# Kernel optimization log

Measured on AMD Instinct MI355X. Metric: run time of the kernel, lower is better.

Reference implementation:

```python
import jax, jax.numpy as jnp
import numpy as np

N_AGENTS = 10
N_ENEMIES = 11
N_ALLIES = 9
H = 64           # rnn_hidden_dim
HYP = 64         # api_hyper_dim
DEPTH = 2        # residual_depth
OWN = 32
EF = 10          # enemy_feats_dim
AF = 10          # ally_feats_dim
N_ACTIONS = 17
BS = 1024


def _hypernet(x, win, bin_, wres, bres, wout, bout):
    # Linear -> ReLU -> DEPTH x (ReLU(Linear)+identity) -> Linear
    h = jax.nn.relu(x @ win + bin_)
    for d in range(DEPTH):
        h = jax.nn.relu(h @ wres[d] + bres[d]) + h
    return h @ wout + bout


def _gru_cell(x, h, wi, wh, bi, bh):
    gi = x @ wi + bi
    gh = h @ wh + bh
    ir, iz, in_ = jnp.split(gi, 3, axis=-1)
    hr, hz, hn = jnp.split(gh, 3, axis=-1)
    r = jax.nn.sigmoid(ir + hr)
    z = jax.nn.sigmoid(iz + hz)
    n = jnp.tanh(in_ + r * hn)
    return (1.0 - z) * n + z * h


def setup_inputs() -> dict:
    key = jax.random.key(0)
    ks = iter(jax.random.split(key, 48))
    def p(shape, s=0.1):
        return jax.random.normal(next(ks), shape, jnp.float32) * s
    N = BS * N_AGENTS
    inp = {
        'own_feats':    p((N, OWN), 1.0),
        'enemy_feats':  p((N * N_ENEMIES, EF), 1.0),
        'ally_feats':   p((N * N_ALLIES, AF), 1.0),
        'hidden_state': p((N, H), 1.0),
        'fc1_w': p((OWN, H)), 'fc1_b': p((H,)),
        'agent_emb': p((N_AGENTS, H)), 'action_emb': p((N_ACTIONS, H)),
        'hen_win': p((EF, HYP)), 'hen_bin': p((HYP,)),
        'hen_wres': p((DEPTH, HYP, HYP)), 'hen_bres': p((DEPTH, HYP)),
        'hen_wout': p((HYP, EF * H)), 'hen_bout': p((EF * H,)),
        'hal_win': p((AF, HYP)), 'hal_bin': p((HYP,)),
        'hal_wres': p((DEPTH, HYP, HYP)), 'hal_bres': p((DEPTH, HYP)),
        'hal_wout': p((HYP, AF * H)), 'hal_bout': p((AF * H,)),
        'gru_wi': p((H, 3 * H)), 'gru_wh': p((H, 3 * H)),
        'gru_bi': p((3 * H,)), 'gru_bh': p((3 * H,)),
        'fc2_w': p((H, 6)), 'fc2_b': p((6,)),
        'how_win': p((EF, HYP)), 'how_bin': p((HYP,)),
        'how_wres': p((DEPTH, HYP, HYP)), 'how_bres': p((DEPTH, HYP)),
        'how_wout': p((HYP, H)), 'how_bout': p((H,)),
        'hob_win': p((EF, HYP)), 'hob_bin': p((HYP,)),
        'hob_wres': p((DEPTH, HYP, HYP)), 'hob_bres': p((DEPTH, HYP)),
        'hob_wout': p((HYP, 1)), 'hob_bout': p((1,)),
        'agent_idx': jax.random.randint(next(ks), (N,), 0, N_AGENTS),
        'last_action_idx': jax.random.randint(next(ks), (N,), 0, N_ACTIONS),
        'bs': BS,
    }
    return inp


def reference(own_feats, enemy_feats, ally_feats, hidden_state,
              fc1_w, fc1_b, agent_emb, action_emb,
              hen_win, hen_bin, hen_wres, hen_bres, hen_wout, hen_bout,
              hal_win, hal_bin, hal_wres, hal_bres, hal_wout, hal_bout,
              gru_wi, gru_wh, gru_bi, gru_bh,
              fc2_w, fc2_b,
              how_win, how_bin, how_wres, how_bres, how_wout, how_bout,
              hob_win, hob_bin, hob_wres, hob_bres, hob_wout, hob_bout,
              agent_idx, last_action_idx, bs):
    N = bs * N_AGENTS
    # own embedding + id embeddings
    emb = own_feats @ fc1_w + fc1_b
    emb = emb + agent_emb[agent_idx] + action_emb[last_action_idx]
    # per-enemy hypernet weights [N*NE, EF, H]; bmm + sum-pool over enemies
    w_en = _hypernet(enemy_feats, hen_win, hen_bin, hen_wres, hen_bres,
                     hen_wout, hen_bout).reshape(-1, EF, H)
    emb_en = jnp.einsum('nf,nfh->nh', enemy_feats, w_en)
    emb_en = emb_en.reshape(N, N_ENEMIES, H).sum(axis=1)
    # per-ally hypernet weights + bmm + sum-pool
    w_al = _hypernet(ally_feats, hal_win, hal_bin, hal_wres, hal_bres,
                     hal_wout, hal_bout).reshape(-1, AF, H)
    emb_al = jnp.einsum('nf,nfh->nh', ally_feats, w_al)
    emb_al = emb_al.reshape(N, N_ALLIES, H).sum(axis=1)
    x = jax.nn.relu(emb + emb_en + emb_al)
    hh = _gru_cell(x, hidden_state.reshape(-1, H), gru_wi, gru_wh, gru_bi, gru_bh)
    q_normal = (hh @ fc2_w + fc2_b).reshape(bs, N_AGENTS, 6)
    # attack-action head: hypernet-generated per-enemy weights/biases
    ow = _hypernet(enemy_feats, how_win, how_bin, how_wres, how_bres,
                   how_wout, how_bout).reshape(N, N_ENEMIES, H)
    ob = _hypernet(enemy_feats, hob_win, hob_bin, hob_wres, hob_bres,
                   hob_wout, hob_bout).reshape(N, N_ENEMIES)
    q_attack = (jnp.einsum('nh,neh->ne', hh, ow) + ob).reshape(bs, N_AGENTS, N_ENEMIES)
    q = jnp.concatenate([q_normal, q_attack], axis=-1)
    return q, hh.reshape(bs, N_AGENTS, H)
```

## Files before the change

### kernel.cpp

```cpp
#include <hip/hip_runtime.h>

#define DI static __device__ __forceinline__

typedef short s16x8 __attribute__((ext_vector_type(8)));
typedef float f32x4 __attribute__((ext_vector_type(4)));
typedef unsigned u32x2 __attribute__((ext_vector_type(2)));

DI unsigned short f2b(float f) {
  union { float f; unsigned u; } v; v.f = f;
  return (unsigned short)((v.u + 0x7FFF + ((v.u >> 16) & 1)) >> 16);
}
DI float b2f(unsigned short s) {
  union { unsigned u; float f; } v; v.u = ((unsigned)s) << 16;
  return v.f;
}
DI unsigned cvtpk(float lo, float hi) {
  unsigned r;
  asm("v_cvt_pk_bf16_f32 %0, %1, %2" : "=v"(r) : "v"(lo), "v"(hi));
  return r;
}
DI f32x4 MFMA(s16x8 a, s16x8 b, f32x4 c) {
  return __builtin_amdgcn_mfma_f32_16x16x32_bf16(a, b, c, 0, 0, 0);
}
DI s16x8 ldg8(const unsigned short* p) { return *(const s16x8*)p; }

#define OFF_WEN   0
#define OFF_WAL   10240
#define OFF_WHOW  20480
#define OFF_WHOB  30720
#define OFF_BGEN  40960
#define OFF_BGAL  83968
#define OFF_WIT   126976
#define OFF_WHT   139264
#define OFF_FC1T  151552
#define OFF_FC2E  153600
#define OFF_HOWT  154624
#define SH_END    159744
#define B_EMB_EN  (SH_END*2)
#define B_EMB_AL  (B_EMB_EN + 2621440)
#define B_HB      (B_EMB_AL + 2621440)
#define B_GBF     (B_HB + 40960)

#define PSTR 680
#define HSTR 72
#define XSTR 40

#define SLOT 28160
#define XBC  5632
DI int xoffc(int row, int b) { return ((row*32  + b) ^ ((row & 7) << 4)); }
DI int hoffc(int row, int b) { return XBC + ((row*128 + b) ^ ((row & 7) << 4)); }

__global__ __launch_bounds__(256) void kprep(
    const float* __restrict__ hen_win, const float* __restrict__ hen_wres,
    const float* __restrict__ hal_win, const float* __restrict__ hal_wres,
    const float* __restrict__ how_win, const float* __restrict__ how_wres,
    const float* __restrict__ hob_win, const float* __restrict__ hob_wres,
    const float* __restrict__ hen_wout, const float* __restrict__ hen_bout,
    const float* __restrict__ hal_wout, const float* __restrict__ hal_bout,
    const float* __restrict__ gru_wi, const float* __restrict__ gru_wh,
    const float* __restrict__ fc1_w, const float* __restrict__ fc2_w,
    const float* __restrict__ how_bout, const float* __restrict__ how_wout,
    unsigned short* __restrict__ ws)
{
  const int gid = blockIdx.x * 256 + threadIdx.x;
  const int gsz = gridDim.x * 256;
  for (int i = gid; i < 4 * 10240; i += gsz) {
    int s = i / 10240, idx = i - s * 10240;
    const float* win  = (s == 0) ? hen_win  : (s == 1) ? hal_win  : (s == 2) ? how_win  : hob_win;
    const float* wres = (s == 0) ? hen_wres : (s == 1) ? hal_wres : (s == 2) ? how_wres : hob_wres;
    float v;
    if (idx < 2048) { int n = idx >> 5, k = idx & 31; v = (k < 10) ? win[k*64 + n] : 0.f; }
    else { int r = idx - 2048; int d = r >> 12; int r2 = r & 4095; int n = r2 >> 6, k = r2 & 63;
           v = wres[d*4096 + k*64 + n]; }
    ws[s * 10240 + idx] = f2b(v);
  }
  for (int i = gid; i < 2 * 43008; i += gsz) {
    int s = i / 43008, idx = i - s * 43008;
    const float* wout = s ? hal_wout : hen_wout;
    const float* bout = s ? hal_bout : hen_bout;
    int kl = idx & 31, n = (idx >> 5) & 63, c = idx >> 11;
    int kfg = c * 32 + kl;
    float v = 0.f;
    if (kfg < 640)      { int k = kfg / 10, f = kfg - k * 10; v = wout[k*640 + f*64 + n]; }
    else if (kfg < 650) { v = bout[(kfg - 640)*64 + n]; }
    ws[(s ? OFF_BGAL : OFF_BGEN) + idx] = f2b(v);
  }
  for (int i = gid; i < 2 * 12288; i += gsz) {
    int s = i / 12288, idx = i - s * 12288;
    int n = idx >> 6, k = idx & 63;
    const float* w = s ? gru_wh : gru_wi;
    ws[(s ? OFF_WHT : OFF_WIT) + idx] = f2b(w[k*192 + n]);
  }
  for (int i = gid; i < 2048; i += gsz) { int n = i >> 5, k = i & 31; ws[OFF_FC1T + i] = f2b(fc1_w[k*64 + n]); }
  for (int i = gid; i < 1024; i += gsz) {
    int n = i >> 6, k = i & 63;
    float v = 0.f; if (n < 6) v = fc2_w[k*6 + n]; else if (n == 6) v = how_bout[k];
    ws[OFF_FC2E + i] = f2b(v);
  }
  for (int i = gid; i < 4096; i += gsz) ws[OFF_HOWT + i] = f2b(how_wout[i]);
}

DI void stage_item(const float* __restrict__ feats, int vrows, char* sl) {
  for (int idx = threadIdx.x; idx < 176*16; idx += 256) {
    int row = idx >> 4, c = idx & 15;
    float v = (row < vrows && c < 10) ? feats[row*10 + c] : 0.f;
    *(unsigned short*)(sl + xoffc(row, c*2)) = f2b(v);
  }
}

DI void stackP(char* sl, int ntiles, const unsigned short* __restrict__ wg,
               const float* __restrict__ bin, const float* __restrict__ bres)
{
  const int l = threadIdx.x & 63, wv = threadIdx.x >> 6;
  const int lrow = l & 15, gq = l >> 4, lk8 = gq * 8;
  const int tis[3] = {wv, wv + 4, wv + 8};
  f32x4 hval[3][4];
  {
    s16x8 wf[4]; f32x4 bv[4];
#pragma unroll
    for (int mt = 0; mt < 4; mt++) {
      wf[mt] = ldg8(wg + (mt*16 + lrow)*32 + lk8);
      bv[mt] = *(const f32x4*)(bin + mt*16 + gq*4);
    }
#pragma unroll
    for (int tt = 0; tt < 3; tt++) {
      if (tis[tt] < ntiles) {
        int row = tis[tt]*16 + lrow;
        s16x8 xf = *(const s16x8*)(sl + xoffc(row, gq*16));
#pragma unroll
        for (int mt = 0; mt < 4; mt++) {
          f32x4 d = MFMA(wf[mt], xf, bv[mt]);
#pragma unroll
          for (int r = 0; r < 4; r++) hval[tt][mt][r] = fmaxf(d[r], 0.f);
          u32x2 pw; pw.x = cvtpk(hval[tt][mt][0], hval[tt][mt][1]);
          pw.y = cvtpk(hval[tt][mt][2], hval[tt][mt][3]);
          *(u32x2*)(sl + hoffc(row, (mt*16 + gq*4)*2)) = pw;
        }
      }
    }
  }
#pragma unroll
  for (int d = 0; d < 2; d++) {
    const unsigned short* wt = wg + 2048 + d * 4096;
    s16x8 wf0[4], wf1[4]; f32x4 bv[4];
#pragma unroll
    for (int mt = 0; mt < 4; mt++) {
      wf0[mt] = ldg8(wt + (mt*16 + lrow)*64 + lk8);
      wf1[mt] = ldg8(wt + (mt*16 + lrow)*64 + 32 + lk8);
      bv[mt] = *(const f32x4*)(bres + d*64 + mt*16 + gq*4);
    }
#pragma unroll
    for (int tt = 0; tt < 3; tt++) {
      if (tis[tt] < ntiles) {
        int row = tis[tt]*16 + lrow;
        s16x8 b0 = *(const s16x8*)(sl + hoffc(row, gq*16));
        s16x8 b1 = *(const s16x8*)(sl + hoffc(row, 64 + gq*16));
#pragma unroll
        for (int mt = 0; mt < 4; mt++) {
          f32x4 acc = MFMA(wf0[mt], b0, bv[mt]);
          acc = MFMA(wf1[mt], b1, acc);
#pragma unroll
          for (int r = 0; r < 4; r++)
            hval[tt][mt][r] = fmaxf(acc[r], 0.f) + hval[tt][mt][r];
          u32x2 pw; pw.x = cvtpk(hval[tt][mt][0], hval[tt][mt][1]);
          pw.y = cvtpk(hval[tt][mt][2], hval[tt][mt][3]);
          *(u32x2*)(sl + hoffc(row, (mt*16 + gq*4)*2)) = pw;
        }
      }
    }
  }
}

__global__ __launch_bounds__(256) void khyp_ea(
    const float* __restrict__ en_feats, const float* __restrict__ al_feats,
    const unsigned short* __restrict__ ws,
    const float* __restrict__ en_bin, const float* __restrict__ en_bres,
    const float* __restrict__ al_bin, const float* __restrict__ al_bres,
    float* __restrict__ emb_en, float* __restrict__ emb_al)
{
  __shared__ __align__(16) char smem[2*SLOT];
  const int t = threadIdx.x;
  const int l = t & 63, wv = t >> 6;
  const int lrow = l & 15, gq = l >> 4, lk8 = gq * 8;

  int its[3]; int nit = 0;
  for (int it = blockIdx.x; it < 1280; it += 512) its[nit++] = it;

  {
    int it0 = its[0];
    const float* f0 = (it0 < 640) ? en_feats + (long)it0*1760
                                  : al_feats + (long)(it0-640)*1440;
    stage_item(f0, (it0 < 640) ? 176 : 144, smem);
  }
  __syncthreads();

  for (int i = 0; i < nit; i++) {
    char* sl = smem + (i & 1) * SLOT;
    const int it = its[i];
    const bool en = it < 640;
    const int E = en ? 11 : 9;
    const float* feats = en ? en_feats + (long)it*1760 : al_feats + (long)(it-640)*1440;
    const unsigned short* Wg = ws + (en ? OFF_WEN : OFF_WAL);
    const unsigned short* Bg = ws + (en ? OFF_BGEN : OFF_BGAL);
    const float* bin  = en ? en_bin  : al_bin;
    const float* bres = en ? en_bres : al_bres;
    float* emb = en ? emb_en + (long)it*1024 : emb_al + (long)(it-640)*1024;

    stackP(sl, E, Wg, bin, bres);
    __syncthreads();

    const int a = t >> 4, kq = t & 15, k0 = kq * 4;
    float acc[4][10];
#pragma unroll
    for (int kk = 0; kk < 4; kk++)
#pragma unroll
      for (int f = 0; f < 10; f++) acc[kk][f] = 0.f;
    for (int e = 0; e < E; e++) {
      int row = a * E + e;
      s16x8 xv8 = *(const s16x8*)(sl + xoffc(row, 0));
      unsigned xv2 = *(const unsigned*)(sl + xoffc(row, 16));
      float xf[10];
#pragma unroll
      for (int f = 0; f < 8; f++) xf[f] = b2f((unsigned short)xv8[f]);
      xf[8] = b2f((unsigned short)(xv2 & 0xFFFF));
      xf[9] = b2f((unsigned short)(xv2 >> 16));
      u32x2 hp = *(const u32x2*)(sl + hoffc(row, k0*2));
      float hf[4] = { b2f((unsigned short)(hp.x & 0xFFFF)), b2f((unsigned short)(hp.x >> 16)),
                      b2f((unsigned short)(hp.y & 0xFFFF)), b2f((unsigned short)(hp.y >> 16)) };
#pragma unroll
      for (int kk = 0; kk < 4; kk++)
#pragma unroll
        for (int f = 0; f < 10; f++) acc[kk][f] += hf[kk] * xf[f];
    }
    float sxv = 0.f; int a2 = 0, fx = 0;
    if (t < 160) {
      a2 = t / 10; fx = t - a2 * 10;
      for (int e = 0; e < E; e++) sxv += feats[(a2*E + e)*10 + fx];
    }
    __syncthreads();

    unsigned short* P2 = (unsigned short*)sl;
    {
      unsigned* Pw = (unsigned*)(P2 + a*PSTR + k0*10);
#pragma unroll
      for (int m = 0; m < 20; m++) {
        const int v0 = 2*m, v1 = 2*m + 1;
        Pw[m] = cvtpk(acc[v0/10][v0%10], acc[v1/10][v1%10]);
      }
    }
    if (t < 160) P2[a2*PSTR + 640 + fx] = f2b(sxv);
    if (t < 352) { int a3 = t / 22, c = t - a3*22; P2[a3*PSTR + 650 + c] = 0; }
    if (i + 1 < nit) {
      int itn = its[i+1];
      const float* fn = (itn < 640) ? en_feats + (long)itn*1760
                                    : al_feats + (long)(itn-640)*1440;
      stage_item(fn, (itn < 640) ? 176 : 144, smem + ((i+1) & 1) * SLOT);
    }
    __syncthreads();

    f32x4 g0 = {0.f,0.f,0.f,0.f}, g1 = {0.f,0.f,0.f,0.f};
    const unsigned short* Bw = Bg + (wv*16 + lrow)*32 + lk8;
#pragma unroll
    for (int c = 0; c < 21; c++) {
      s16x8 af = *(const s16x8*)&P2[lrow*PSTR + c*32 + lk8];
      s16x8 bf = ldg8(Bw + c*2048);
      if (c & 1) g1 = MFMA(af, bf, g1); else g0 = MFMA(af, bf, g0);
    }
#pragma unroll
    for (int r = 0; r < 4; r++)
      emb[(gq*4 + r)*64 + wv*16 + lrow] = g0[r] + g1[r];
  }
}

__global__ __launch_bounds__(256) void kfused(
    const float* __restrict__ own, const float* __restrict__ agent_emb,
    const float* __restrict__ action_emb,
    const int* __restrict__ agent_idx, const int* __restrict__ last_action,
    const float* __restrict__ emb_en, const float* __restrict__ emb_al,
    const float* __restrict__ hidden,
    const unsigned short* __restrict__ ws,
    const float* __restrict__ fc1_b, const float* __restrict__ bi,
    const float* __restrict__ bh, const float* __restrict__ fc2_b,
    float* __restrict__ qout, float* __restrict__ hhout,
    unsigned short* __restrict__ g_bf, float* __restrict__ hb)
{
  __shared__ unsigned short own_lds[16*32];
  __shared__ unsigned short x_lds[16*HSTR];
  __shared__ unsigned short hp_lds[16*HSTR];
  __shared__ unsigned short hh_lds[16*HSTR];
  const int t = threadIdx.x;
  const int l = t & 63, wv = t >> 6;
  const int lrow = l & 15, lk8 = (l >> 4) * 8, lr4 = (l >> 4) * 4;
  const int n0 = blockIdx.x * 16;

  const unsigned short* fc1T = ws + OFF_FC1T;
  const unsigned short* wiT  = ws + OFF_WIT;
  const unsigned short* whT  = ws + OFF_WHT;
  const unsigned short* howT = ws + OFF_HOWT;
  const unsigned short* fc2e = ws + OFF_FC2E;

  for (int i = t; i < 512; i += 256) own_lds[i] = f2b(own[n0*32 + i]);
  for (int i = t; i < 1024; i += 256) hp_lds[(i >> 6)*HSTR + (i & 63)] = f2b(hidden[n0*64 + i]);
  __syncthreads();

  const int j = wv * 16 + lrow;
  {
    s16x8 a0 = *(const s16x8*)&own_lds[lrow*32 + lk8];
    s16x8 b0 = ldg8(fc1T + (wv*16 + lrow)*32 + lk8);
    f32x4 c0 = MFMA(a0, b0, f32x4{0.f,0.f,0.f,0.f});
    float fb = fc1_b[j];
#pragma unroll
    for (int r = 0; r < 4; r++) {
      int aa = lr4 + r; int n = n0 + aa;
      int ai = agent_idx[n], la = last_action[n];
      float v = c0[r] + fb + agent_emb[ai*64 + j] + action_emb[la*64 + j]
              + emb_en[(long)n*64 + j] + emb_al[(long)n*64 + j];
      x_lds[aa*HSTR + j] = f2b(fmaxf(v, 0.f));
    }
  }
  __syncthreads();

  {
    s16x8 xa[2], ha[2];
#pragma unroll
    for (int s = 0; s < 2; s++) {
      xa[s] = *(const s16x8*)&x_lds[lrow*HSTR + s*32 + lk8];
      ha[s] = *(const s16x8*)&hp_lds[lrow*HSTR + s*32 + lk8];
    }
    f32x4 gi[3], gh[3];
#pragma unroll
    for (int g3 = 0; g3 < 3; g3++) { gi[g3] = f32x4{0.f,0.f,0.f,0.f}; gh[g3] = f32x4{0.f,0.f,0.f,0.f}; }
#pragma unroll
    for (int g3 = 0; g3 < 3; g3++) {
      int tl = wv + g3 * 4;
#pragma unroll
      for (int s = 0; s < 2; s++) {
        gi[g3] = MFMA(xa[s], ldg8(wiT + (tl*16 + lrow)*64 + s*32 + lk8), gi[g3]);
        gh[g3] = MFMA(ha[s], ldg8(whT + (tl*16 + lrow)*64 + s*32 + lk8), gh[g3]);
      }
    }
    float bir = bi[j], biz = bi[64 + j], bin_ = bi[128 + j];
    float bhr = bh[j], bhz = bh[64 + j], bhn = bh[128 + j];
#pragma unroll
    for (int r = 0; r < 4; r++) {
      int aa = lr4 + r; int n = n0 + aa;
      float rr = 1.f / (1.f + __expf(-(gi[0][r] + bir + gh[0][r] + bhr)));
      float zz = 1.f / (1.f + __expf(-(gi[1][r] + biz + gh[1][r] + bhz)));
      float nn = tanhf(gi[2][r] + bin_ + rr * (gh[2][r] + bhn));
      float hp = hidden[n*64 + j];
      float hhv = (1.f - zz) * nn + zz * hp;
      hhout[n*64 + j] = hhv;
      hh_lds[aa*HSTR + j] = f2b(hhv);
    }
  }
  __syncthreads();

  {
    s16x8 hha[2];
#pragma unroll
    for (int s = 0; s < 2; s++) hha[s] = *(const s16x8*)&hh_lds[lrow*HSTR + s*32 + lk8];
    f32x4 gc = {0.f,0.f,0.f,0.f};
#pragma unroll
    for (int s = 0; s < 2; s++) gc = MFMA(hha[s], ldg8(howT + (wv*16 + lrow)*64 + s*32 + lk8), gc);
#pragma unroll
    for (int r = 0; r < 4; r++) g_bf[(n0 + lr4 + r)*64 + wv*16 + lrow] = f2b(gc[r]);
    if (wv == 0) {
      f32x4 qc = {0.f,0.f,0.f,0.f};
#pragma unroll
      for (int s = 0; s < 2; s++) qc = MFMA(hha[s], ldg8(fc2e + lrow*64 + s*32 + lk8), qc);
#pragma unroll
      for (int r = 0; r < 4; r++) {
        int n = n0 + lr4 + r;
        if (lrow < 6)       qout[n*17 + lrow] = qc[r] + fc2_b[lrow];
        else if (lrow == 6) hb[n] = qc[r];
      }
    }
  }
}

template<int TMAX, bool WLAST>
DI void stack_batch(const unsigned short* __restrict__ x_lds,
                    unsigned short* const (&hbp)[TMAX], const int (&tis)[TMAX], int NT,
                    const unsigned short* __restrict__ wg,
                    const float* __restrict__ bin, const float* __restrict__ bres,
                    f32x4 (&hval)[TMAX][4])
{
  const int l = threadIdx.x & 63;
  const int lrow = l & 15, gq = l >> 4, lk8 = gq * 8;
  {
    s16x8 wf[4]; f32x4 bv[4];
#pragma unroll
    for (int mt = 0; mt < 4; mt++) {
      wf[mt] = ldg8(wg + (mt*16 + lrow)*32 + lk8);
      bv[mt] = *(const f32x4*)(bin + mt*16 + gq*4);
    }
#pragma unroll
    for (int tt = 0; tt < TMAX; tt++) {
      if (tis[tt] < NT) {
        s16x8 xf = *(const s16x8*)&x_lds[(tis[tt]*16 + lrow)*XSTR + lk8];
#pragma unroll
        for (int mt = 0; mt < 4; mt++) {
          f32x4 d = MFMA(wf[mt], xf, bv[mt]);
#pragma unroll
          for (int r = 0; r < 4; r++) hval[tt][mt][r] = fmaxf(d[r], 0.f);
        }
        unsigned short* wr = hbp[tt] + lrow*HSTR;
#pragma unroll
        for (int mt = 0; mt < 4; mt++) {
          u32x2 pw;
          pw.x = cvtpk(hval[tt][mt][0], hval[tt][mt][1]);
          pw.y = cvtpk(hval[tt][mt][2], hval[tt][mt][3]);
          *(u32x2*)&wr[mt*16 + gq*4] = pw;
        }
      }
    }
  }
#pragma unroll
  for (int d = 0; d < 2; d++) {
    const unsigned short* wt = wg + 2048 + d * 4096;
    s16x8 wf[4][2]; f32x4 bv[4];
#pragma unroll
    for (int mt = 0; mt < 4; mt++) {
      wf[mt][0] = ldg8(wt + (mt*16 + lrow)*64 + lk8);
      wf[mt][1] = ldg8(wt + (mt*16 + lrow)*64 + 32 + lk8);
      bv[mt] = *(const f32x4*)(bres + d*64 + mt*16 + gq*4);
    }
#pragma unroll
    for (int tt = 0; tt < TMAX; tt++) {
      if (tis[tt] < NT) {
        const unsigned short* hr = hbp[tt] + lrow*HSTR;
        s16x8 b0 = *(const s16x8*)&hr[lk8];
        s16x8 b1 = *(const s16x8*)&hr[32 + lk8];
#pragma unroll
        for (int mt = 0; mt < 4; mt++) {
          f32x4 a = MFMA(wf[mt][0], b0, bv[mt]);
          a = MFMA(wf[mt][1], b1, a);
#pragma unroll
          for (int r = 0; r < 4; r++)
            hval[tt][mt][r] = fmaxf(a[r], 0.f) + hval[tt][mt][r];
        }
        if (d == 0 || WLAST) {
          unsigned short* wr = hbp[tt] + lrow*HSTR;
#pragma unroll
          for (int mt = 0; mt < 4; mt++) {
            u32x2 pw;
            pw.x = cvtpk(hval[tt][mt][0], hval[tt][mt][1]);
            pw.y = cvtpk(hval[tt][mt][2], hval[tt][mt][3]);
            *(u32x2*)&wr[mt*16 + gq*4] = pw;
          }
        }
      }
    }
  }
}

__global__ __launch_bounds__(256) void kattack(
    const float* __restrict__ en_feats, const unsigned short* __restrict__ ws,
    const float* __restrict__ how_bin, const float* __restrict__ how_bres,
    const float* __restrict__ hob_bin, const float* __restrict__ hob_bres,
    const unsigned short* __restrict__ g_bf, const float* __restrict__ hbuf,
    const float* __restrict__ hob_wout, const float* __restrict__ hob_bout,
    float* __restrict__ qout)
{
  __shared__ __align__(16) char smem[41728];
  unsigned short* x_lds = (unsigned short*)smem;
  unsigned short* scr   = (unsigned short*)(smem + 14080);
  const int t = threadIdx.x;
  const int l = t & 63, wv = t >> 6;
  const int lrow = l & 15, gq = l >> 4;
  const int blk = blockIdx.x;
  const float* feats = en_feats + (long)blk * 1760;

  for (int idx = t; idx < 176*32; idx += 256) {
    int row = idx >> 5, c = idx & 31;
    x_lds[row*XSTR + c] = (c < 10) ? f2b(feats[row*10 + c]) : (unsigned short)0;
  }
  __syncthreads();

  int tis[3] = {wv, wv + 4, wv + 8};
  unsigned short* hbp[3] = { scr + (wv*3+0)*16*HSTR, scr + (wv*3+1)*16*HSTR, scr + (wv*3+2)*16*HSTR };
  f32x4 hval[3][4];

  stack_batch<3, false>(x_lds, hbp, tis, 11, ws + OFF_WHOB, hob_bin, hob_bres, hval);
  f32x4 hw[4];
#pragma unroll
  for (int mt = 0; mt < 4; mt++) hw[mt] = *(const f32x4*)(hob_wout + mt*16 + gq*4);
  float qbv[3] = {0.f, 0.f, 0.f};
#pragma unroll
  for (int tt = 0; tt < 3; tt++) {
    if (tis[tt] < 11) {
      float s = 0.f;
#pragma unroll
      for (int mt = 0; mt < 4; mt++)
#pragma unroll
        for (int r = 0; r < 4; r++) s += hval[tt][mt][r] * hw[mt][r];
      s += __shfl_xor(s, 16, 64);
      s += __shfl_xor(s, 32, 64);
      qbv[tt] = s;
    }
  }

  stack_batch<3, false>(x_lds, hbp, tis, 11, ws + OFF_WHOW, how_bin, how_bres, hval);
  const float hob_b0 = hob_bout[0];
#pragma unroll
  for (int tt = 0; tt < 3; tt++) {
    if (tis[tt] < 11) {
      int row = tis[tt]*16 + lrow;
      unsigned ag = (unsigned)row / 11u;
      int n = blk*16 + (int)ag;
      float s = 0.f;
#pragma unroll
      for (int mt = 0; mt < 4; mt++) {
        u32x2 gv = *(const u32x2*)(g_bf + (long)n*64 + mt*16 + gq*4);
        s += hval[tt][mt][0] * b2f((unsigned short)(gv.x & 0xFFFF))
           + hval[tt][mt][1] * b2f((unsigned short)(gv.x >> 16))
           + hval[tt][mt][2] * b2f((unsigned short)(gv.y & 0xFFFF))
           + hval[tt][mt][3] * b2f((unsigned short)(gv.y >> 16));
      }
      s += __shfl_xor(s, 16, 64);
      s += __shfl_xor(s, 32, 64);
      if (l < 16) {
        int e = row - (int)ag * 11;
        qout[n*17 + 6 + e] = s + qbv[tt] + hbuf[n] + hob_b0;
      }
    }
  }
}

extern "C" void kernel_launch(void* const* d_in, const int* in_sizes, int n_in,
                              void* d_out, int out_size, void* d_ws, size_t ws_size,
                              hipStream_t stream)
{
  (void)in_sizes; (void)n_in; (void)out_size; (void)ws_size;
  const float* own        = (const float*)d_in[0];
  const float* enemy      = (const float*)d_in[1];
  const float* ally       = (const float*)d_in[2];
  const float* hidden     = (const float*)d_in[3];
  const float* fc1_w      = (const float*)d_in[4];
  const float* fc1_b      = (const float*)d_in[5];
  const float* agent_emb  = (const float*)d_in[6];
  const float* action_emb = (const float*)d_in[7];
  const float* hen_win  = (const float*)d_in[8];  const float* hen_bin  = (const float*)d_in[9];
  const float* hen_wres = (const float*)d_in[10]; const float* hen_bres = (const float*)d_in[11];
  const float* hen_wout = (const float*)d_in[12]; const float* hen_bout = (const float*)d_in[13];
  const float* hal_win  = (const float*)d_in[14]; const float* hal_bin  = (const float*)d_in[15];
  const float* hal_wres = (const float*)d_in[16]; const float* hal_bres = (const float*)d_in[17];
  const float* hal_wout = (const float*)d_in[18]; const float* hal_bout = (const float*)d_in[19];
  const float* gru_wi = (const float*)d_in[20];   const float* gru_wh = (const float*)d_in[21];
  const float* gru_bi = (const float*)d_in[22];   const float* gru_bh = (const float*)d_in[23];
  const float* fc2_w  = (const float*)d_in[24];   const float* fc2_b  = (const float*)d_in[25];
  const float* how_win  = (const float*)d_in[26]; const float* how_bin  = (const float*)d_in[27];
  const float* how_wres = (const float*)d_in[28]; const float* how_bres = (const float*)d_in[29];
  const float* how_wout = (const float*)d_in[30]; const float* how_bout = (const float*)d_in[31];
  const float* hob_win  = (const float*)d_in[32]; const float* hob_bin  = (const float*)d_in[33];
  const float* hob_wres = (const float*)d_in[34]; const float* hob_bres = (const float*)d_in[35];
  const float* hob_wout = (const float*)d_in[36]; const float* hob_bout = (const float*)d_in[37];
  const int* agent_idx   = (const int*)d_in[38];
  const int* last_action = (const int*)d_in[39];

  unsigned short* ws = (unsigned short*)d_ws;
  float* emb_en = (float*)((char*)d_ws + B_EMB_EN);
  float* emb_al = (float*)((char*)d_ws + B_EMB_AL);
  float* hb     = (float*)((char*)d_ws + B_HB);
  unsigned short* g_bf = (unsigned short*)((char*)d_ws + B_GBF);

  float* q  = (float*)d_out;
  float* hh = q + 1024*10*17;

  kprep<<<128, 256, 0, stream>>>(hen_win, hen_wres, hal_win, hal_wres,
      how_win, how_wres, hob_win, hob_wres,
      hen_wout, hen_bout, hal_wout, hal_bout,
      gru_wi, gru_wh, fc1_w, fc2_w, how_bout, how_wout, ws);
  khyp_ea<<<512, 256, 0, stream>>>(enemy, ally, ws,
      hen_bin, hen_bres, hal_bin, hal_bres, emb_en, emb_al);
  kfused<<<640, 256, 0, stream>>>(own, agent_emb, action_emb, agent_idx, last_action,
      emb_en, emb_al, hidden, ws, fc1_b, gru_bi, gru_bh, fc2_b, q, hh, g_bf, hb);
  kattack<<<640, 256, 0, stream>>>(enemy, ws, how_bin, how_bres, hob_bin, hob_bres,
      g_bf, hb, hob_wout, hob_bout, q);
}
```

Measured before the change: 78.05 us.

## Process two fixed items per block in khyp_ea, sharing weight fragments

The khyp_ea kernel changes from a grid-stride loop over 1280 items with 512 blocks (unbalanced: 2 or 3 items per block) to 640 blocks that each handle exactly two items of the same type, enemy or ally. Each hypernet weight fragment is loaded once and applied to both items, and the final 21-step MFMA loop reuses each B fragment for two accumulators. The cost is more live registers (hval doubled) and the loss of overlap between staging the next item and computing the current one.

```diff
diff --git a/kernel.cpp b/kernel.cpp
--- a/kernel.cpp
+++ b/kernel.cpp
@@ -108,67 +108,54 @@
   }
 }
 
-DI void stackP(char* sl, int ntiles, const unsigned short* __restrict__ wg,
-               const float* __restrict__ bin, const float* __restrict__ bres)
-{
-  const int l = threadIdx.x & 63, wv = threadIdx.x >> 6;
-  const int lrow = l & 15, gq = l >> 4, lk8 = gq * 8;
-  const int tis[3] = {wv, wv + 4, wv + 8};
-  f32x4 hval[3][4];
-  {
-    s16x8 wf[4]; f32x4 bv[4];
-#pragma unroll
-    for (int mt = 0; mt < 4; mt++) {
-      wf[mt] = ldg8(wg + (mt*16 + lrow)*32 + lk8);
-      bv[mt] = *(const f32x4*)(bin + mt*16 + gq*4);
-    }
-#pragma unroll
-    for (int tt = 0; tt < 3; tt++) {
-      if (tis[tt] < ntiles) {
-        int row = tis[tt]*16 + lrow;
-        s16x8 xf = *(const s16x8*)(sl + xoffc(row, gq*16));
-#pragma unroll
-        for (int mt = 0; mt < 4; mt++) {
-          f32x4 d = MFMA(wf[mt], xf, bv[mt]);
-#pragma unroll
-          for (int r = 0; r < 4; r++) hval[tt][mt][r] = fmaxf(d[r], 0.f);
-          u32x2 pw; pw.x = cvtpk(hval[tt][mt][0], hval[tt][mt][1]);
-          pw.y = cvtpk(hval[tt][mt][2], hval[tt][mt][3]);
-          *(u32x2*)(sl + hoffc(row, (mt*16 + gq*4)*2)) = pw;
-        }
-      }
-    }
-  }
-#pragma unroll
-  for (int d = 0; d < 2; d++) {
-    const unsigned short* wt = wg + 2048 + d * 4096;
-    s16x8 wf0[4], wf1[4]; f32x4 bv[4];
-#pragma unroll
-    for (int mt = 0; mt < 4; mt++) {
-      wf0[mt] = ldg8(wt + (mt*16 + lrow)*64 + lk8);
-      wf1[mt] = ldg8(wt + (mt*16 + lrow)*64 + 32 + lk8);
-      bv[mt] = *(const f32x4*)(bres + d*64 + mt*16 + gq*4);
-    }
-#pragma unroll
-    for (int tt = 0; tt < 3; tt++) {
-      if (tis[tt] < ntiles) {
-        int row = tis[tt]*16 + lrow;
-        s16x8 b0 = *(const s16x8*)(sl + hoffc(row, gq*16));
-        s16x8 b1 = *(const s16x8*)(sl + hoffc(row, 64 + gq*16));
-#pragma unroll
-        for (int mt = 0; mt < 4; mt++) {
-          f32x4 acc = MFMA(wf0[mt], b0, bv[mt]);
-          acc = MFMA(wf1[mt], b1, acc);
-#pragma unroll
-          for (int r = 0; r < 4; r++)
-            hval[tt][mt][r] = fmaxf(acc[r], 0.f) + hval[tt][mt][r];
-          u32x2 pw; pw.x = cvtpk(hval[tt][mt][0], hval[tt][mt][1]);
-          pw.y = cvtpk(hval[tt][mt][2], hval[tt][mt][3]);
-          *(u32x2*)(sl + hoffc(row, (mt*16 + gq*4)*2)) = pw;
-        }
-      }
-    }
-  }
+DI void pbuild_acc(const char* sl, int E, float (&acc)[4][10]) {
+  const int t = threadIdx.x;
+  const int a = t >> 4, k0 = (t & 15) * 4;
+#pragma unroll
+  for (int kk = 0; kk < 4; kk++)
+#pragma unroll
+    for (int f = 0; f < 10; f++) acc[kk][f] = 0.f;
+  for (int e = 0; e < E; e++) {
+    int row = a * E + e;
+    s16x8 xv8 = *(const s16x8*)(sl + xoffc(row, 0));
+    unsigned xv2 = *(const unsigned*)(sl + xoffc(row, 16));
+    float xf[10];
+#pragma unroll
+    for (int f = 0; f < 8; f++) xf[f] = b2f((unsigned short)xv8[f]);
+    xf[8] = b2f((unsigned short)(xv2 & 0xFFFF));
+    xf[9] = b2f((unsigned short)(xv2 >> 16));
+    u32x2 hp = *(const u32x2*)(sl + hoffc(row, k0*2));
+    float hf[4] = { b2f((unsigned short)(hp.x & 0xFFFF)), b2f((unsigned short)(hp.x >> 16)),
+                    b2f((unsigned short)(hp.y & 0xFFFF)), b2f((unsigned short)(hp.y >> 16)) };
+#pragma unroll
+    for (int kk = 0; kk < 4; kk++)
+#pragma unroll
+      for (int f = 0; f < 10; f++) acc[kk][f] += hf[kk] * xf[f];
+  }
+}
+
+DI void pbuild_write(unsigned short* P2, const float (&acc)[4][10], float sxv, int E,
+                     const float* __restrict__ feats) {
+  const int t = threadIdx.x;
+  const int a = t >> 4, k0 = (t & 15) * 4;
+  unsigned* Pw = (unsigned*)(P2 + a*PSTR + k0*10);
+#pragma unroll
+  for (int m = 0; m < 20; m++) {
+    const int v0 = 2*m, v1 = 2*m + 1;
+    Pw[m] = cvtpk(acc[v0/10][v0%10], acc[v1/10][v1%10]);
+  }
+  if (t < 160) { int a2 = t / 10, fx = t - a2*10; P2[a2*PSTR + 640 + fx] = f2b(sxv); }
+  if (t < 352) { int a3 = t / 22, c = t - a3*22; P2[a3*PSTR + 650 + c] = 0; }
+}
+
+DI float sx_of(const float* __restrict__ feats, int E) {
+  const int t = threadIdx.x;
+  float s = 0.f;
+  if (t < 160) {
+    int a2 = t / 10, fx = t - a2 * 10;
+    for (int e = 0; e < E; e++) s += feats[(a2*E + e)*10 + fx];
+  }
+  return s;
 }
 
 __global__ __launch_bounds__(256) void khyp_ea(
@@ -183,92 +170,119 @@
   const int l = t & 63, wv = t >> 6;
   const int lrow = l & 15, gq = l >> 4, lk8 = gq * 8;
 
-  int its[3]; int nit = 0;
-  for (int it = blockIdx.x; it < 1280; it += 512) its[nit++] = it;
-
+  const bool en = blockIdx.x < 320;
+  const int i0 = en ? blockIdx.x * 2 : (blockIdx.x - 320) * 2;
+  const int E = en ? 11 : 9;
+  const int rows = E * 16;
+  const float* feats0 = (en ? en_feats : al_feats) + (long)i0 * rows * 10;
+  const float* feats1 = feats0 + rows * 10;
+  const unsigned short* Wg = ws + (en ? OFF_WEN : OFF_WAL);
+  const unsigned short* Bg = ws + (en ? OFF_BGEN : OFF_BGAL);
+  const float* bin  = en ? en_bin  : al_bin;
+  const float* bres = en ? en_bres : al_bres;
+  float* emb0 = (en ? emb_en : emb_al) + (long)i0 * 1024;
+  float* emb1 = emb0 + 1024;
+
+  stage_item(feats0, rows, smem);
+  stage_item(feats1, rows, smem + SLOT);
+  __syncthreads();
+
+  const int tis[3] = {wv, wv + 4, wv + 8};
+  f32x4 hval[2][3][4];
   {
-    int it0 = its[0];
-    const float* f0 = (it0 < 640) ? en_feats + (long)it0*1760
-                                  : al_feats + (long)(it0-640)*1440;
-    stage_item(f0, (it0 < 640) ? 176 : 144, smem);
-  }
-  __syncthreads();
-
-  for (int i = 0; i < nit; i++) {
-    char* sl = smem + (i & 1) * SLOT;
-    const int it = its[i];
-    const bool en = it < 640;
-    const int E = en ? 11 : 9;
-    const float* feats = en ? en_feats + (long)it*1760 : al_feats + (long)(it-640)*1440;
-    const unsigned short* Wg = ws + (en ? OFF_WEN : OFF_WAL);
-    const unsigned short* Bg = ws + (en ? OFF_BGEN : OFF_BGAL);
-    const float* bin  = en ? en_bin  : al_bin;
-    const float* bres = en ? en_bres : al_bres;
-    float* emb = en ? emb_en + (long)it*1024 : emb_al + (long)(it-640)*1024;
-
-    stackP(sl, E, Wg, bin, bres);
-    __syncthreads();
-
-    const int a = t >> 4, kq = t & 15, k0 = kq * 4;
-    float acc[4][10];
-#pragma unroll
-    for (int kk = 0; kk < 4; kk++)
-#pragma unroll
-      for (int f = 0; f < 10; f++) acc[kk][f] = 0.f;
-    for (int e = 0; e < E; e++) {
-      int row = a * E + e;
-      s16x8 xv8 = *(const s16x8*)(sl + xoffc(row, 0));
-      unsigned xv2 = *(const unsigned*)(sl + xoffc(row, 16));
-      float xf[10];
-#pragma unroll
-      for (int f = 0; f < 8; f++) xf[f] = b2f((unsigned short)xv8[f]);
-      xf[8] = b2f((unsigned short)(xv2 & 0xFFFF));
-      xf[9] = b2f((unsigned short)(xv2 >> 16));
-      u32x2 hp = *(const u32x2*)(sl + hoffc(row, k0*2));
-      float hf[4] = { b2f((unsigned short)(hp.x & 0xFFFF)), b2f((unsigned short)(hp.x >> 16)),
-                      b2f((unsigned short)(hp.y & 0xFFFF)), b2f((unsigned short)(hp.y >> 16)) };
-#pragma unroll
-      for (int kk = 0; kk < 4; kk++)
-#pragma unroll
-        for (int f = 0; f < 10; f++) acc[kk][f] += hf[kk] * xf[f];
-    }
-    float sxv = 0.f; int a2 = 0, fx = 0;
-    if (t < 160) {
-      a2 = t / 10; fx = t - a2 * 10;
-      for (int e = 0; e < E; e++) sxv += feats[(a2*E + e)*10 + fx];
-    }
-    __syncthreads();
-
-    unsigned short* P2 = (unsigned short*)sl;
-    {
-      unsigned* Pw = (unsigned*)(P2 + a*PSTR + k0*10);
-#pragma unroll
-      for (int m = 0; m < 20; m++) {
-        const int v0 = 2*m, v1 = 2*m + 1;
-        Pw[m] = cvtpk(acc[v0/10][v0%10], acc[v1/10][v1%10]);
-      }
-    }
-    if (t < 160) P2[a2*PSTR + 640 + fx] = f2b(sxv);
-    if (t < 352) { int a3 = t / 22, c = t - a3*22; P2[a3*PSTR + 650 + c] = 0; }
-    if (i + 1 < nit) {
-      int itn = its[i+1];
-      const float* fn = (itn < 640) ? en_feats + (long)itn*1760
-                                    : al_feats + (long)(itn-640)*1440;
-      stage_item(fn, (itn < 640) ? 176 : 144, smem + ((i+1) & 1) * SLOT);
-    }
-    __syncthreads();
-
-    f32x4 g0 = {0.f,0.f,0.f,0.f}, g1 = {0.f,0.f,0.f,0.f};
-    const unsigned short* Bw = Bg + (wv*16 + lrow)*32 + lk8;
-#pragma unroll
-    for (int c = 0; c < 21; c++) {
-      s16x8 af = *(const s16x8*)&P2[lrow*PSTR + c*32 + lk8];
-      s16x8 bf = ldg8(Bw + c*2048);
-      if (c & 1) g1 = MFMA(af, bf, g1); else g0 = MFMA(af, bf, g0);
-    }
-#pragma unroll
-    for (int r = 0; r < 4; r++)
-      emb[(gq*4 + r)*64 + wv*16 + lrow] = g0[r] + g1[r];
+    s16x8 wf[4]; f32x4 bv[4];
+#pragma unroll
+    for (int mt = 0; mt < 4; mt++) {
+      wf[mt] = ldg8(Wg + (mt*16 + lrow)*32 + lk8);
+      bv[mt] = *(const f32x4*)(bin + mt*16 + gq*4);
+    }
+#pragma unroll
+    for (int ss = 0; ss < 2; ss++) {
+      char* sl = smem + ss * SLOT;
+#pragma unroll
+      for (int tt = 0; tt < 3; tt++) {
+        if (tis[tt] < E) {
+          int row = tis[tt]*16 + lrow;
+          s16x8 xf = *(const s16x8*)(sl + xoffc(row, gq*16));
+#pragma unroll
+          for (int mt = 0; mt < 4; mt++) {
+            f32x4 d = MFMA(wf[mt], xf, bv[mt]);
+#pragma unroll
+            for (int r = 0; r < 4; r++) hval[ss][tt][mt][r] = fmaxf(d[r], 0.f);
+            u32x2 pw; pw.x = cvtpk(hval[ss][tt][mt][0], hval[ss][tt][mt][1]);
+            pw.y = cvtpk(hval[ss][tt][mt][2], hval[ss][tt][mt][3]);
+            *(u32x2*)(sl + hoffc(row, (mt*16 + gq*4)*2)) = pw;
+          }
+        }
+      }
+    }
+  }
+#pragma unroll
+  for (int d = 0; d < 2; d++) {
+    const unsigned short* wt = Wg + 2048 + d * 4096;
+    s16x8 wf0[4], wf1[4]; f32x4 bv[4];
+#pragma unroll
+    for (int mt = 0; mt < 4; mt++) {
+      wf0[mt] = ldg8(wt + (mt*16 + lrow)*64 + lk8);
+      wf1[mt] = ldg8(wt + (mt*16 + lrow)*64 + 32 + lk8);
+      bv[mt] = *(const f32x4*)(bres + d*64 + mt*16 + gq*4);
+    }
+#pragma unroll
+    for (int ss = 0; ss < 2; ss++) {
+      char* sl = smem + ss * SLOT;
+#pragma unroll
+      for (int tt = 0; tt < 3; tt++) {
+        if (tis[tt] < E) {
+          int row = tis[tt]*16 + lrow;
+          s16x8 b0 = *(const s16x8*)(sl + hoffc(row, gq*16));
+          s16x8 b1 = *(const s16x8*)(sl + hoffc(row, 64 + gq*16));
+#pragma unroll
+          for (int mt = 0; mt < 4; mt++) {
+            f32x4 a = MFMA(wf0[mt], b0, bv[mt]);
+            a = MFMA(wf1[mt], b1, a);
+#pragma unroll
+            for (int r = 0; r < 4; r++)
+              hval[ss][tt][mt][r] = fmaxf(a[r], 0.f) + hval[ss][tt][mt][r];
+            u32x2 pw; pw.x = cvtpk(hval[ss][tt][mt][0], hval[ss][tt][mt][1]);
+            pw.y = cvtpk(hval[ss][tt][mt][2], hval[ss][tt][mt][3]);
+            *(u32x2*)(sl + hoffc(row, (mt*16 + gq*4)*2)) = pw;
+          }
+        }
+      }
+    }
+  }
+  __syncthreads();
+
+  float acc[4][10];
+  pbuild_acc(smem, E, acc);
+  float sx0 = sx_of(feats0, E);
+  __syncthreads();
+
+  pbuild_write((unsigned short*)smem, acc, sx0, E, feats0);
+  pbuild_acc(smem + SLOT, E, acc);
+  float sx1 = sx_of(feats1, E);
+  __syncthreads();
+
+  pbuild_write((unsigned short*)(smem + SLOT), acc, sx1, E, feats1);
+  __syncthreads();
+
+  unsigned short* P0 = (unsigned short*)smem;
+  unsigned short* P1 = (unsigned short*)(smem + SLOT);
+  f32x4 a00 = {0.f,0.f,0.f,0.f}, a01 = {0.f,0.f,0.f,0.f};
+  f32x4 a10 = {0.f,0.f,0.f,0.f}, a11 = {0.f,0.f,0.f,0.f};
+  const unsigned short* Bw = Bg + (wv*16 + lrow)*32 + lk8;
+#pragma unroll
+  for (int c = 0; c < 21; c++) {
+    s16x8 bf = ldg8(Bw + c*2048);
+    s16x8 af0 = *(const s16x8*)&P0[lrow*PSTR + c*32 + lk8];
+    s16x8 af1 = *(const s16x8*)&P1[lrow*PSTR + c*32 + lk8];
+    if (c & 1) { a01 = MFMA(af0, bf, a01); a11 = MFMA(af1, bf, a11); }
+    else       { a00 = MFMA(af0, bf, a00); a10 = MFMA(af1, bf, a10); }
+  }
+#pragma unroll
+  for (int r = 0; r < 4; r++) {
+    emb0[(gq*4 + r)*64 + wv*16 + lrow] = a00[r] + a01[r];
+    emb1[(gq*4 + r)*64 + wv*16 + lrow] = a10[r] + a11[r];
   }
 }
 
@@ -571,7 +585,7 @@
       how_win, how_wres, hob_win, hob_wres,
       hen_wout, hen_bout, hal_wout, hal_bout,
       gru_wi, gru_wh, fc1_w, fc2_w, how_bout, how_wout, ws);
-  khyp_ea<<<512, 256, 0, stream>>>(enemy, ally, ws,
+  khyp_ea<<<640, 256, 0, stream>>>(enemy, ally, ws,
       hen_bin, hen_bres, hal_bin, hal_bres, emb_en, emb_al);
   kfused<<<640, 256, 0, stream>>>(own, agent_emb, action_emb, agent_idx, last_action,
       emb_en, emb_al, hidden, ws, fc1_b, gru_bi, gru_bh, fc2_b, q, hh, g_bf, hb);
```

Measured after the change: 84.15 us. 7.8% more time.
